# Optimization experiments

Measured on AMD Instinct MI355X. Metric: run time of the kernel, lower is better.

## Reference

```python
import jax, jax.numpy as jnp
import numpy as np

K = 1024
H = 16

def setup_inputs() -> dict:
    key = jax.random.key(0)
    ks = jax.random.split(key, 6)
    s = 1.0 / np.sqrt(K)
    return {
        "x": jax.random.normal(ks[0], (2, 2048, K), dtype=jnp.float32),
        "Wq": jax.random.uniform(ks[1], (K, K), jnp.float32, -s, s),
        "Wk": jax.random.uniform(ks[2], (K, K), jnp.float32, -s, s),
        "Wv": jax.random.uniform(ks[3], (K, K), jnp.float32, -s, s),
        "Wu": jax.random.uniform(ks[4], (K, K), jnp.float32, -s, s),
        "bu": jax.random.uniform(ks[5], (K,), jnp.float32, -s, s),
    }

def reference(x, Wq, Wk, Wv, Wu, bu):
    b, t, k = x.shape
    hd = k // H  # head dim = 64
    scale = jnp.asarray(k, x.dtype) ** 0.25  # Bloem-style: scale q and k each by k^(1/4)
    # nn.Linear(bias=False): y = x @ W.T
    q = (jnp.einsum('btk,ok->bto', x, Wq) / scale).reshape(b, t, H, hd)
    kk = (jnp.einsum('btk,ok->bto', x, Wk) / scale).reshape(b, t, H, hd)
    v = jnp.einsum('btk,ok->bto', x, Wv).reshape(b, t, H, hd)
    dot = jnp.einsum('bthd,bshd->bhts', q, kk)  # [b,h,t,t]
    att = jax.nn.softmax(dot, axis=-1)
    out = jnp.einsum('bhts,bshd->bthd', att, v).reshape(b, t, k)
    return jnp.einsum('btk,ok->bto', out, Wu) + bu
```

## Files before the change

### kernel.cpp

```cpp
#include <hip/hip_runtime.h>

typedef __bf16 bf16;
typedef bf16  bf16x8 __attribute__((ext_vector_type(8)));
typedef bf16  bf16x4 __attribute__((ext_vector_type(4)));
typedef float f32x4  __attribute__((ext_vector_type(4)));
typedef unsigned int u32x2 __attribute__((ext_vector_type(2)));
typedef unsigned int u32x4 __attribute__((ext_vector_type(4)));

#define MFMA16(a, b, c) __builtin_amdgcn_mfma_f32_16x16x32_bf16((a), (b), (c), 0, 0, 0)
#define AS1 __attribute__((address_space(1)))
#define AS3 __attribute__((address_space(3)))

__device__ __forceinline__ void gld_lds16(const bf16* g, bf16* l) {
    __builtin_amdgcn_global_load_lds((AS1 void*)(g), (AS3 void*)(l), 16, 0, 0);
}


__global__ __launch_bounds__(256) void cvt_all(const float* __restrict__ x,
                                               const float* __restrict__ Wq, const float* __restrict__ Wk,
                                               const float* __restrict__ Wv, const float* __restrict__ Wu,
                                               bf16* ox, bf16* oq, bf16* ok, bf16* ov, bf16* ou,
                                               float sq, float sk) {
    int bid = blockIdx.x;
    const float* src; bf16* dst; float sc; int base;
    if (bid < 4096) { src = x; dst = ox; sc = 1.0f; base = bid; }
    else {
        int w = (bid - 4096) >> 10; base = (bid - 4096) & 1023;
        switch (w) {
            case 0:  src = Wq; dst = oq; sc = sq;   break;
            case 1:  src = Wk; dst = ok; sc = sk;   break;
            case 2:  src = Wv; dst = ov; sc = 1.0f; break;
            default: src = Wu; dst = ou; sc = 1.0f; break;
        }
    }
    int idx = (base * 256 + threadIdx.x) * 4;
    float4 v = *(const float4*)(src + idx);
    bf16x4 o;
    o[0] = (bf16)(v.x * sc); o[1] = (bf16)(v.y * sc);
    o[2] = (bf16)(v.z * sc); o[3] = (bf16)(v.w * sc);
    *(bf16x4*)(dst + idx) = o;
}

__device__ __forceinline__ void gemm_core(const bf16* __restrict__ A, const bf16* __restrict__ B,
                                          int mBase, int nBase, bf16* As, bf16* Bs,
                                          f32x4 acc[4][4]) {
    const int tid = threadIdx.x;
    const int wave = tid >> 6, lane = tid & 63;
    const int g = lane >> 4, lr = lane & 15;
    const int wm = (wave & 1) << 6, wn = (wave >> 1) << 6;
    const int q = lane >> 2;
    const int cswz = ((lane & 3) ^ ((lane >> 3) & 3)) << 3;
    const int pcs  = (g ^ ((lr >> 1) & 3)) << 3;

    const int rb0 = wave << 4, rb1 = rb0 + 64;
    const bf16* a0 = A + (size_t)(mBase + rb0 + q) * 1024 + cswz;
    const bf16* a1 = A + (size_t)(mBase + rb1 + q) * 1024 + cswz;
    const bf16* b0 = B + (size_t)(nBase + rb0 + q) * 1024 + cswz;
    const bf16* b1 = B + (size_t)(nBase + rb1 + q) * 1024 + cswz;

    gld_lds16(a0, As + rb0 * 32);
    gld_lds16(a1, As + rb1 * 32);
    gld_lds16(b0, Bs + rb0 * 32);
    gld_lds16(b1, Bs + rb1 * 32);
    __syncthreads();

    for (int k0 = 0; k0 < 1024; k0 += 32) {
        const int cur = (k0 >> 5) & 1;
        bf16* Asc = As + cur * (128 * 32);
        bf16* Bsc = Bs + cur * (128 * 32);
        if (k0 + 32 < 1024) {
            bf16* Asn = As + (cur ^ 1) * (128 * 32);
            bf16* Bsn = Bs + (cur ^ 1) * (128 * 32);
            gld_lds16(a0 + k0 + 32, Asn + rb0 * 32);
            gld_lds16(a1 + k0 + 32, Asn + rb1 * 32);
            gld_lds16(b0 + k0 + 32, Bsn + rb0 * 32);
            gld_lds16(b1 + k0 + 32, Bsn + rb1 * 32);
        }

        bf16x8 af[4], bfr[4];
#pragma unroll
        for (int i = 0; i < 4; i++)
            af[i] = *(const bf16x8*)&Asc[(wm + (i << 4) + lr) * 32 + pcs];
#pragma unroll
        for (int j = 0; j < 4; j++)
            bfr[j] = *(const bf16x8*)&Bsc[(wn + (j << 4) + lr) * 32 + pcs];
#pragma unroll
        for (int i = 0; i < 4; i++)
#pragma unroll
            for (int j = 0; j < 4; j++)
                acc[i][j] = MFMA16(af[i], bfr[j], acc[i][j]);

        __syncthreads();
    }
}

__device__ __forceinline__ void stage_tile16(const bf16* G, int k0, bf16* Ls,
                                             int wave, int q, int cswz) {
#pragma unroll
    for (int c = 0; c < 2; c++) {
        int rb = c * 8 + wave;
        gld_lds16(G + (size_t)(rb * 16 + q) * 1024 + k0 + cswz, Ls + rb * 16 * 32);
    }
}

__global__ __launch_bounds__(512, 2) void gemm_qkv(const bf16* __restrict__ X,
                                                   const bf16* __restrict__ Wqk,
                                                   const bf16* __restrict__ Wv,
                                                   bf16* __restrict__ Qo, bf16* __restrict__ Ko,
                                                   bf16* __restrict__ Vto) {
    __shared__ bf16 As[2][256][32];
    __shared__ bf16 Bs[2][256][32];
    const int tid = threadIdx.x;
    const int wave = tid >> 6, lane = tid & 63;
    const int g = lane >> 4, lr = lane & 15;
    const int q = lane >> 2;
    const int cswz = ((lane & 3) ^ ((lane >> 3) & 3)) << 3;
    const int pcs  = (g ^ ((lr >> 1) & 3)) << 3;
    const int wm = wave >> 2, wn = wave & 3;

    const int bid = blockIdx.x;
    const bool qk = bid < 128;
    int mBase, nBase;
    const bf16 *Ap, *Bp;
    if (qk) { mBase = (bid >> 4) << 8; nBase = (bid & 15) << 8; Ap = Wqk; Bp = X; }
    else    { int v = bid - 128; mBase = (v >> 2) << 8; nBase = (v & 3) << 8; Ap = X; Bp = Wv; }

    const bf16* Ag = Ap + (size_t)mBase * 1024;
    const bf16* Bg = Bp + (size_t)nBase * 1024;

    f32x4 acc[8][4] = {};

    stage_tile16(Ag, 0, &As[0][0][0], wave, q, cswz);
    stage_tile16(Bg, 0, &Bs[0][0][0], wave, q, cswz);
    __syncthreads();

    for (int t = 0; t < 32; t++) {
        const int k0 = t << 5;
        bf16* Ac = &As[t & 1][0][0];
        bf16* Bc = &Bs[t & 1][0][0];
        const bool pre = (t < 31);

        bf16x8 bfr[4], af[4];
#pragma unroll
        for (int j = 0; j < 4; j++)
            bfr[j] = *(const bf16x8*)&Bc[(wn * 64 + (j << 4) + lr) * 32 + pcs];
#pragma unroll
        for (int i = 0; i < 4; i++)
            af[i] = *(const bf16x8*)&Ac[(wm * 128 + (i << 4) + lr) * 32 + pcs];
        if (pre) stage_tile16(Ag, k0 + 32, &As[(t & 1) ^ 1][0][0], wave, q, cswz);
        __builtin_amdgcn_s_barrier();
        __builtin_amdgcn_s_setprio(1);
#pragma unroll
        for (int i = 0; i < 4; i++)
#pragma unroll
            for (int j = 0; j < 4; j++)
                acc[i][j] = MFMA16(af[i], bfr[j], acc[i][j]);
        __builtin_amdgcn_s_setprio(0);

#pragma unroll
        for (int i = 0; i < 4; i++)
            af[i] = *(const bf16x8*)&Ac[(wm * 128 + 64 + (i << 4) + lr) * 32 + pcs];
        if (pre) stage_tile16(Bg, k0 + 32, &Bs[(t & 1) ^ 1][0][0], wave, q, cswz);
        __builtin_amdgcn_s_barrier();
        __builtin_amdgcn_s_setprio(1);
#pragma unroll
        for (int i = 0; i < 4; i++)
#pragma unroll
            for (int j = 0; j < 4; j++)
                acc[4 + i][j] = MFMA16(af[i], bfr[j], acc[4 + i][j]);
        __builtin_amdgcn_s_setprio(0);

        __syncthreads();
    }

    if (qk) {
#pragma unroll
        for (int i = 0; i < 8; i++) {
            int m0 = mBase + wm * 128 + (i << 4) + (g << 2);
            bf16* dst = (m0 >> 10) ? Ko : Qo;
            int feat = m0 & 1023;
            int h = feat >> 6, d = feat & 63;
#pragma unroll
            for (int j = 0; j < 4; j++) {
                int tt = nBase + wn * 64 + (j << 4) + lr;
                int b = tt >> 11, tl = tt & 2047;
                bf16x4 v;
#pragma unroll
                for (int r = 0; r < 4; r++) v[r] = (bf16)acc[i][j][r];
                *(bf16x4*)&dst[(((size_t)((b << 4) + h) * 2048 + tl) << 6) + d] = v;
            }
        }
    } else {
#pragma unroll
        for (int i = 0; i < 8; i++) {
            int t0 = mBase + wm * 128 + (i << 4) + (g << 2);
            int b = t0 >> 11, tl = t0 & 2047;
#pragma unroll
            for (int j = 0; j < 4; j++) {
                int o = nBase + wn * 64 + (j << 4) + lr;
                int h = o >> 6, d = o & 63;
                bf16x4 v;
#pragma unroll
                for (int r = 0; r < 4; r++) v[r] = (bf16)acc[i][j][r];
                *(bf16x4*)&Vto[((size_t)(((b << 4) + h) << 6) + d) * 2048 + tl] = v;
            }
        }
    }
}

__global__ __launch_bounds__(256) void gemm_out(const bf16* __restrict__ Wu, const bf16* __restrict__ A,
                                                const float* __restrict__ bias, float* __restrict__ out) {
    __shared__ bf16 As[2][128 * 32];
    __shared__ bf16 Bs[2][128 * 32];
    const int tid = threadIdx.x;
    const int wave = tid >> 6, lane = tid & 63;
    const int g = lane >> 4, lr = lane & 15;
    const int wm = (wave & 1) << 6, wn = (wave >> 1) << 6;
    const int mBase = blockIdx.y * 128, nBase = blockIdx.x * 128;

    f32x4 acc[4][4] = {};
    gemm_core(Wu, A, mBase, nBase, &As[0][0], &Bs[0][0], acc);

#pragma unroll
    for (int i = 0; i < 4; i++) {
        int o = mBase + wm + (i << 4) + (g << 2);
        float4 bv = *(const float4*)&bias[o];
#pragma unroll
        for (int j = 0; j < 4; j++) {
            int t = nBase + wn + (j << 4) + lr;
            float4 v;
            v.x = acc[i][j][0] + bv.x;
            v.y = acc[i][j][1] + bv.y;
            v.z = acc[i][j][2] + bv.z;
            v.w = acc[i][j][3] + bv.w;
            *(float4*)&out[((size_t)t << 10) + o] = v;
        }
    }
}

__global__ __launch_bounds__(256, 4) void attn(const bf16* __restrict__ Q, const bf16* __restrict__ Kt,
                                               const bf16* __restrict__ Vt, bf16* __restrict__ O) {
    __shared__ bf16 Qs[2][64][32];
    __shared__ bf16 Ks[2][128][32];
    __shared__ bf16 Vs[4][64][32];

    const int tid = threadIdx.x;
    const int wave = tid >> 6, lane = tid & 63;
    const int g = lane >> 4, lr = lane & 15;
    const int q = lane >> 2;
    const int cswz = ((lane & 3) ^ ((lane >> 3) & 3)) << 3;
    const int pcs  = (g ^ ((lr >> 1) & 3)) << 3;
    const int pair = wave >> 1;
    const int shalf = wave & 1;

    const int bid = blockIdx.x;
    const int bh = ((bid & 7) << 2) | (bid >> 8);
    const int qBase = ((bid >> 3) & 31) << 6;

    const bf16* Qg = Q + ((size_t)bh * 2048 + qBase) * 64;
    const bf16* Kg = Kt + (size_t)bh * 2048 * 64;
    const bf16* Vg = Vt + (size_t)bh * 64 * 2048;

#pragma unroll
    for (int i = 0; i < 2; i++) {
        int bi = (wave << 1) + i;
        int p = bi >> 2, rb = (bi & 3) << 4;
        gld_lds16(Qg + (rb + q) * 64 + (p << 5) + cswz, &Qs[p][rb][0]);
    }
    __syncthreads();

    bf16x8 qf[2][2];
#pragma unroll
    for (int ks = 0; ks < 2; ks++)
#pragma unroll
        for (int tt = 0; tt < 2; tt++)
            qf[ks][tt] = *(const bf16x8*)&Qs[ks][(pair << 5) + (tt << 4) + lr][pcs];

    bf16x8 ones;
#pragma unroll
    for (int i = 0; i < 8; i++) ones[i] = (bf16)1.0f;

    f32x4 oacc[2][4] = {};
    f32x4 oaccL[2] = {};

    for (int s0 = 0; s0 < 2048; s0 += 128) {
        __syncthreads();
#pragma unroll
        for (int i = 0; i < 4; i++) {
            int bi = (wave << 2) + i;
            {
                int p = bi >> 3, rb = (bi & 7) << 4;
                gld_lds16(Kg + (size_t)(s0 + rb + q) * 64 + (p << 5) + cswz, &Ks[p][rb][0]);
            }
            {
                int p = bi >> 2, rb = (bi & 3) << 4;
                gld_lds16(Vg + (size_t)(rb + q) * 2048 + s0 + (p << 5) + cswz, &Vs[p][rb][0]);
            }
        }
        __syncthreads();

#pragma unroll
        for (int sblk = 0; sblk < 2; sblk++) {
            f32x4 sacc[2][2] = {};
#pragma unroll
            for (int ks = 0; ks < 2; ks++)
#pragma unroll
                for (int isub = 0; isub < 2; isub++) {
                    bf16x8 kf = *(const bf16x8*)
                        &Ks[ks][(shalf << 6) + (sblk << 5) + (isub << 4) + lr][pcs];
                    sacc[isub][0] = MFMA16(kf, qf[ks][0], sacc[isub][0]);
                    sacc[isub][1] = MFMA16(kf, qf[ks][1], sacc[isub][1]);
                }
            bf16x8 pf[2];
#pragma unroll
            for (int tt = 0; tt < 2; tt++) {
                bf16x4 e0, e1;
#pragma unroll
                for (int r = 0; r < 4; r++) {
                    e0[r] = (bf16)__builtin_amdgcn_exp2f(sacc[0][tt][r]);
                    e1[r] = (bf16)__builtin_amdgcn_exp2f(sacc[1][tt][r]);
                }
                u32x2 a = __builtin_bit_cast(u32x2, e0);
                u32x2 b = __builtin_bit_cast(u32x2, e1);
                u32x2 t0  = __builtin_amdgcn_permlane32_swap(a.x, b.x, false, false);
                u32x2 w02 = __builtin_amdgcn_permlane16_swap(t0.x, t0.y, false, false);
                u32x2 t1  = __builtin_amdgcn_permlane32_swap(a.y, b.y, false, false);
                u32x2 w13 = __builtin_amdgcn_permlane16_swap(t1.x, t1.y, false, false);
                u32x4 w = {w02.x, w13.x, w02.y, w13.y};
                pf[tt] = __builtin_bit_cast(bf16x8, w);
            }
#pragma unroll
            for (int jd = 0; jd < 4; jd++) {
                bf16x8 vf = *(const bf16x8*)&Vs[(shalf << 1) + sblk][(jd << 4) + lr][pcs];
                oacc[0][jd] = MFMA16(pf[0], vf, oacc[0][jd]);
                oacc[1][jd] = MFMA16(pf[1], vf, oacc[1][jd]);
            }
            oaccL[0] = MFMA16(pf[0], ones, oaccL[0]);
            oaccL[1] = MFMA16(pf[1], ones, oaccL[1]);
        }
    }

    __syncthreads();
    float* Odump = (float*)&Ks[0][0][0];
    float* Ldump = (float*)&Vs[0][0][0];
    if (shalf == 1) {
#pragma unroll
        for (int tt = 0; tt < 2; tt++) {
#pragma unroll
            for (int jd = 0; jd < 4; jd++)
                *(f32x4*)&Odump[(pair << 11) + (((tt << 2) + jd) << 8) + (lane << 2)] = oacc[tt][jd];
            *(f32x4*)&Ldump[(pair << 9) + (tt << 8) + (lane << 2)] = oaccL[tt];
        }
    }
    __syncthreads();
    if (shalf == 0) {
        const int b = bh >> 4, h = bh & 15;
#pragma unroll
        for (int tt = 0; tt < 2; tt++) {
            f32x4 Lp = *(const f32x4*)&Ldump[(pair << 9) + (tt << 8) + (lane << 2)];
            f32x4 Ls = oaccL[tt] + Lp;
            float linv[4];
#pragma unroll
            for (int r = 0; r < 4; r++) linv[r] = 1.0f / Ls[r];
#pragma unroll
            for (int jd = 0; jd < 4; jd++) {
                f32x4 Op = *(const f32x4*)&Odump[(pair << 11) + (((tt << 2) + jd) << 8) + (lane << 2)];
                f32x4 v = oacc[tt][jd] + Op;
#pragma unroll
                for (int r = 0; r < 4; r++) {
                    int t = qBase + (pair << 5) + (tt << 4) + (g << 2) + r;
                    int col = (h << 6) + (jd << 4) + lr;
                    O[(((size_t)(b * 2048 + t)) << 10) + col] = (bf16)(v[r] * linv[r]);
                }
            }
        }
    }
}

extern "C" void kernel_launch(void* const* d_in, const int* in_sizes, int n_in,
                              void* d_out, int out_size, void* d_ws, size_t ws_size,
                              hipStream_t stream) {
    const float* x  = (const float*)d_in[0];
    const float* Wq = (const float*)d_in[1];
    const float* Wk = (const float*)d_in[2];
    const float* Wv = (const float*)d_in[3];
    const float* Wu = (const float*)d_in[4];
    const float* bu = (const float*)d_in[5];
    float* out = (float*)d_out;

    char* ws = (char*)d_ws;
    bf16* xbf  = (bf16*)(ws);
    bf16* wqbf = (bf16*)(ws + ((size_t)8  << 20));
    bf16* wkbf = (bf16*)(ws + ((size_t)10 << 20));
    bf16* wvbf = (bf16*)(ws + ((size_t)12 << 20));
    bf16* wubf = (bf16*)(ws + ((size_t)14 << 20));
    bf16* Qb   = (bf16*)(ws + ((size_t)16 << 20));
    bf16* Kb   = (bf16*)(ws + ((size_t)24 << 20));
    bf16* Vtb  = (bf16*)(ws + ((size_t)32 << 20));
    bf16* attnO = xbf;

    const float iscale_k = 0.17677669529663687f;
    const float iscale_q = 0.25503540109f;

    cvt_all<<<8192, 256, 0, stream>>>(x, Wq, Wk, Wv, Wu, xbf, wqbf, wkbf, wvbf, wubf,
                                      iscale_q, iscale_k);

    gemm_qkv<<<dim3(192), 512, 0, stream>>>(xbf, wqbf, wvbf, Qb, Kb, Vtb);
    attn<<<dim3(1024), 256, 0, stream>>>(Qb, Kb, Vtb, attnO);
    gemm_out<<<dim3(32, 8), 256, 0, stream>>>(wubf, attnO, bu, out);
}
```

Baseline: 185.0 us.

## Triple-buffer QKV GEMM prefetch and single-buffer the output GEMM

The QKV projection GEMM now uses three LDS stages, prefetching two K-steps ahead. Per-iteration __syncthreads is replaced with explicit vmcnt waits plus barriers, and launch bounds drop to one block per SM. The output GEMM core drops its double buffering in favour of a synchronous load-then-compute loop with a single LDS buffer. The aim is to hide more global latency in the QKV GEMM, at the cost of lower occupancy there and exposed load latency in the output GEMM.

```diff
diff --git a/kernel.cpp b/kernel.cpp
--- a/kernel.cpp
+++ b/kernel.cpp
@@ -58,44 +58,31 @@
     const bf16* b0 = B + (size_t)(nBase + rb0 + q) * 1024 + cswz;
     const bf16* b1 = B + (size_t)(nBase + rb1 + q) * 1024 + cswz;
 
-    gld_lds16(a0, As + rb0 * 32);
-    gld_lds16(a1, As + rb1 * 32);
-    gld_lds16(b0, Bs + rb0 * 32);
-    gld_lds16(b1, Bs + rb1 * 32);
-    __syncthreads();
-
     for (int k0 = 0; k0 < 1024; k0 += 32) {
-        const int cur = (k0 >> 5) & 1;
-        bf16* Asc = As + cur * (128 * 32);
-        bf16* Bsc = Bs + cur * (128 * 32);
-        if (k0 + 32 < 1024) {
-            bf16* Asn = As + (cur ^ 1) * (128 * 32);
-            bf16* Bsn = Bs + (cur ^ 1) * (128 * 32);
-            gld_lds16(a0 + k0 + 32, Asn + rb0 * 32);
-            gld_lds16(a1 + k0 + 32, Asn + rb1 * 32);
-            gld_lds16(b0 + k0 + 32, Bsn + rb0 * 32);
-            gld_lds16(b1 + k0 + 32, Bsn + rb1 * 32);
-        }
+        __syncthreads();
+        gld_lds16(a0 + k0, As + rb0 * 32);
+        gld_lds16(a1 + k0, As + rb1 * 32);
+        gld_lds16(b0 + k0, Bs + rb0 * 32);
+        gld_lds16(b1 + k0, Bs + rb1 * 32);
+        __syncthreads();
 
         bf16x8 af[4], bfr[4];
 #pragma unroll
         for (int i = 0; i < 4; i++)
-            af[i] = *(const bf16x8*)&Asc[(wm + (i << 4) + lr) * 32 + pcs];
+            af[i] = *(const bf16x8*)&As[(wm + (i << 4) + lr) * 32 + pcs];
 #pragma unroll
         for (int j = 0; j < 4; j++)
-            bfr[j] = *(const bf16x8*)&Bsc[(wn + (j << 4) + lr) * 32 + pcs];
+            bfr[j] = *(const bf16x8*)&Bs[(wn + (j << 4) + lr) * 32 + pcs];
 #pragma unroll
         for (int i = 0; i < 4; i++)
 #pragma unroll
             for (int j = 0; j < 4; j++)
                 acc[i][j] = MFMA16(af[i], bfr[j], acc[i][j]);
-
-        __syncthreads();
-    }
-}
-
-__device__ __forceinline__ void stage_tile16(const bf16* G, int k0, bf16* Ls,
-                                             int wave, int q, int cswz) {
+    }
+}
+
+__device__ __forceinline__ void stage_tile(const bf16* G, int k0, bf16* Ls,
+                                           int wave, int q, int cswz) {
 #pragma unroll
     for (int c = 0; c < 2; c++) {
         int rb = c * 8 + wave;
@@ -103,13 +90,13 @@
     }
 }
 
-__global__ __launch_bounds__(512, 2) void gemm_qkv(const bf16* __restrict__ X,
+__global__ __launch_bounds__(512, 1) void gemm_qkv(const bf16* __restrict__ X,
                                                    const bf16* __restrict__ Wqk,
                                                    const bf16* __restrict__ Wv,
                                                    bf16* __restrict__ Qo, bf16* __restrict__ Ko,
                                                    bf16* __restrict__ Vto) {
-    __shared__ bf16 As[2][256][32];
-    __shared__ bf16 Bs[2][256][32];
+    __shared__ bf16 As[3][256 * 32];
+    __shared__ bf16 Bs[3][256 * 32];
     const int tid = threadIdx.x;
     const int wave = tid >> 6, lane = tid & 63;
     const int g = lane >> 4, lr = lane & 15;
@@ -130,15 +117,20 @@
 
     f32x4 acc[8][4] = {};
 
-    stage_tile16(Ag, 0, &As[0][0][0], wave, q, cswz);
-    stage_tile16(Bg, 0, &Bs[0][0][0], wave, q, cswz);
-    __syncthreads();
-
+    stage_tile(Ag, 0,  &As[0][0], wave, q, cswz);
+    stage_tile(Bg, 0,  &Bs[0][0], wave, q, cswz);
+    stage_tile(Ag, 32, &As[1][0], wave, q, cswz);
+    stage_tile(Bg, 32, &Bs[1][0], wave, q, cswz);
+    asm volatile("s_waitcnt vmcnt(4)" ::: "memory");
+    __builtin_amdgcn_s_barrier();
+
+    int cur = 0;
     for (int t = 0; t < 32; t++) {
-        const int k0 = t << 5;
-        bf16* Ac = &As[t & 1][0][0];
-        bf16* Bc = &Bs[t & 1][0][0];
-        const bool pre = (t < 31);
+        bf16* Ac = &As[cur][0];
+        bf16* Bc = &Bs[cur][0];
+        const int nx2 = (cur >= 1) ? cur - 1 : 2;
+        const int k2 = (t + 2) << 5;
+        const bool pre = (t < 30);
 
         bf16x8 bfr[4], af[4];
 #pragma unroll
@@ -147,7 +139,7 @@
 #pragma unroll
         for (int i = 0; i < 4; i++)
             af[i] = *(const bf16x8*)&Ac[(wm * 128 + (i << 4) + lr) * 32 + pcs];
-        if (pre) stage_tile16(Ag, k0 + 32, &As[(t & 1) ^ 1][0][0], wave, q, cswz);
+        if (pre) stage_tile(Ag, k2, &As[nx2][0], wave, q, cswz);
         __builtin_amdgcn_s_barrier();
         __builtin_amdgcn_s_setprio(1);
 #pragma unroll
@@ -160,7 +152,7 @@
 #pragma unroll
         for (int i = 0; i < 4; i++)
             af[i] = *(const bf16x8*)&Ac[(wm * 128 + 64 + (i << 4) + lr) * 32 + pcs];
-        if (pre) stage_tile16(Bg, k0 + 32, &Bs[(t & 1) ^ 1][0][0], wave, q, cswz);
+        if (pre) stage_tile(Bg, k2, &Bs[nx2][0], wave, q, cswz);
         __builtin_amdgcn_s_barrier();
         __builtin_amdgcn_s_setprio(1);
 #pragma unroll
@@ -170,7 +162,10 @@
                 acc[4 + i][j] = MFMA16(af[i], bfr[j], acc[4 + i][j]);
         __builtin_amdgcn_s_setprio(0);
 
-        __syncthreads();
+        if (pre) asm volatile("s_waitcnt vmcnt(4)" ::: "memory");
+        else     asm volatile("s_waitcnt vmcnt(0)" ::: "memory");
+        __builtin_amdgcn_s_barrier();
+        cur = (cur >= 2) ? 0 : cur + 1;
     }
 
     if (qk) {
@@ -210,8 +205,8 @@
 
 __global__ __launch_bounds__(256) void gemm_out(const bf16* __restrict__ Wu, const bf16* __restrict__ A,
                                                 const float* __restrict__ bias, float* __restrict__ out) {
-    __shared__ bf16 As[2][128 * 32];
-    __shared__ bf16 Bs[2][128 * 32];
+    __shared__ bf16 As[128 * 32];
+    __shared__ bf16 Bs[128 * 32];
     const int tid = threadIdx.x;
     const int wave = tid >> 6, lane = tid & 63;
     const int g = lane >> 4, lr = lane & 15;
@@ -219,7 +214,7 @@
     const int mBase = blockIdx.y * 128, nBase = blockIdx.x * 128;
 
     f32x4 acc[4][4] = {};
-    gemm_core(Wu, A, mBase, nBase, &As[0][0], &Bs[0][0], acc);
+    gemm_core(Wu, A, mBase, nBase, As, Bs, acc);
 
 #pragma unroll
     for (int i = 0; i < 4; i++) {
```

Result: slower. 189.0 us (+2.1%).
